# Performance work log

Measured on AMD Instinct MI355X. Metric: run time of the kernel, lower is better.

## Reference

```python
import jax, jax.numpy as jnp
import numpy as np

N_NODES = 50000
N_EDGES = 800000
NUM_GRAPHS = 1024
IN_DIM = 25
DIM = 64
STEPS = 3


def setup_inputs() -> dict:
    key = jax.random.key(0)
    ks = jax.random.split(key, 16)
    s = 0.1
    return {
        "x": jax.random.normal(ks[0], (N_NODES, IN_DIM), dtype=jnp.float32),
        "edge_index": jax.random.randint(ks[1], (2, N_EDGES), 0, N_NODES),
        "batch": jnp.sort(jax.random.randint(ks[2], (N_NODES,), 0, NUM_GRAPHS)),
        "W0": jax.random.normal(ks[3], (IN_DIM, DIM), dtype=jnp.float32) * s,
        "b0": jnp.zeros((DIM,), jnp.float32),
        "Wc": jax.random.normal(ks[4], (DIM, DIM), dtype=jnp.float32) * s,
        "bc": jnp.zeros((DIM,), jnp.float32),
        "Wih": jax.random.normal(ks[5], (4 * DIM, 2 * DIM), dtype=jnp.float32) * s,
        "Whh": jax.random.normal(ks[6], (4 * DIM, DIM), dtype=jnp.float32) * s,
        "bih": jnp.zeros((4 * DIM,), jnp.float32),
        "bhh": jnp.zeros((4 * DIM,), jnp.float32),
        "W1": jax.random.normal(ks[7], (2 * DIM, DIM), dtype=jnp.float32) * s,
        "b1": jnp.zeros((DIM,), jnp.float32),
        "W2": jax.random.normal(ks[8], (DIM, 1), dtype=jnp.float32) * s,
        "b2": jnp.zeros((1,), jnp.float32),
    }


def _lstm_cell(xin, h, c, Wih, Whh, bih, bhh):
    gates = xin @ Wih.T + h @ Whh.T + bih + bhh  # [B, 4*DIM]
    i, f, g, o = jnp.split(gates, 4, axis=-1)
    i, f, o = jax.nn.sigmoid(i), jax.nn.sigmoid(f), jax.nn.sigmoid(o)
    g = jnp.tanh(g)
    c = f * c + i * g
    h = o * jnp.tanh(c)
    return h, c


def reference(x, edge_index, batch, W0, b0, Wc, bc, Wih, Whh, bih, bhh, W1, b1, W2, b2):
    n = x.shape[0]
    # lin0 + relu
    h = jax.nn.relu(x @ W0 + b0)
    # GCNConv: x @ W, add self loops, symmetric normalization, scatter-add
    hw = h @ Wc
    loops = jnp.arange(n, dtype=edge_index.dtype)
    row = jnp.concatenate([edge_index[0], loops])  # sources
    col = jnp.concatenate([edge_index[1], loops])  # targets
    deg = jax.ops.segment_sum(jnp.ones_like(row, dtype=hw.dtype), col, num_segments=n)
    dinv = jnp.where(deg > 0, jax.lax.rsqrt(deg), 0.0)
    norm = dinv[row] * dinv[col]
    msg = hw[row] * norm[:, None]  # [E+N, DIM] gather
    agg = jax.ops.segment_sum(msg, col, num_segments=n) + bc
    h = jax.nn.relu(agg)
    # Set2Set pooling with LSTM, 3 processing steps
    B = NUM_GRAPHS
    q_star = jnp.zeros((B, 2 * DIM), h.dtype)
    hs = jnp.zeros((B, DIM), h.dtype)
    cs = jnp.zeros((B, DIM), h.dtype)
    for _ in range(STEPS):
        hs, cs = _lstm_cell(q_star, hs, cs, Wih, Whh, bih, bhh)
        q = hs  # [B, DIM]
        e = jnp.sum(h * q[batch], axis=-1)  # [N]
        emax = jax.ops.segment_max(e, batch, num_segments=B)
        a = jnp.exp(e - emax[batch])
        asum = jax.ops.segment_sum(a, batch, num_segments=B)
        a = a / asum[batch]
        r = jax.ops.segment_sum(a[:, None] * h, batch, num_segments=B)  # [B, DIM]
        q_star = jnp.concatenate([q, r], axis=-1)
    out = jax.nn.relu(q_star @ W1 + b1)
    out = out @ W2 + b2
    return out.reshape(-1)
```

## Files before the change

### kernel.cpp

```cpp
#include <hip/hip_runtime.h>
#include <hip/hip_fp16.h>
#include <math.h>

#define N_NODES 50000
#define N_EDGES 800000
#define NGRAPH  1024
#define IN_DIM  25
#define DIM     64

#define NBK 98
#define CAP 12288
#define NPB 128
#define NFILL (NBK * 4)
#define NBIN 391

__device__ inline float wsum(float v) {
#pragma unroll
  for (int off = 32; off > 0; off >>= 1) v += __shfl_xor(v, off, 64);
  return v;
}
__device__ inline int wsumi(int v) {
#pragma unroll
  for (int off = 32; off > 0; off >>= 1) v += __shfl_xor(v, off, 64);
  return v;
}
__device__ inline float sigmoidf(float x) { return 1.f / (1.f + expf(-x)); }

__global__ __launch_bounds__(256) void k_bin(const int* __restrict__ ei,
    int* __restrict__ gcur, int* __restrict__ pairs,
    const float* __restrict__ Wih, const float* __restrict__ Whh,
    float* __restrict__ WT) {
  __shared__ int lcnt[NBK];
  __shared__ int lbase[NBK];
  int t = threadIdx.x;
  if (blockIdx.x == NBIN) {
    for (int i = t; i < 3 * DIM * 4 * DIM; i += 256) {
      int k = i >> 8, tt = i & 255;
      WT[i] = (k < 2 * DIM) ? Wih[tt * 2 * DIM + k] : Whh[tt * DIM + (k - 2 * DIM)];
    }
    return;
  }
  int base = blockIdx.x * 2048;
  for (int i = t; i < NBK; i += 256) lcnt[i] = 0;
  __syncthreads();
  int rows[8], cols[8], rank[8];
#pragma unroll
  for (int k = 0; k < 8; k++) {
    int e = base + k * 256 + t;
    if (e < N_EDGES) {
      rows[k] = ei[e];
      cols[k] = ei[N_EDGES + e];
      rank[k] = atomicAdd(&lcnt[cols[k] >> 9], 1);
    } else {
      cols[k] = -1;
    }
  }
  __syncthreads();
  for (int i = t; i < NBK; i += 256)
    lbase[i] = lcnt[i] ? atomicAdd(&gcur[i], lcnt[i]) : 0;
  __syncthreads();
#pragma unroll
  for (int k = 0; k < 8; k++) {
    if (cols[k] >= 0) {
      int bkt = cols[k] >> 9;
      int pos = lbase[bkt] + rank[k];
      if (pos < CAP)
        pairs[(size_t)bkt * CAP + pos] = ((cols[k] & 511) << 16) | rows[k];
    }
  }
}

__global__ __launch_bounds__(256) void k_lin0(const float* __restrict__ x,
    const float* __restrict__ W0, const float* __restrict__ b0,
    const float* __restrict__ Wc, __half* __restrict__ hw16) {
  __shared__ float sx[64][IN_DIM + 1];
  __shared__ float sW0[IN_DIM][DIM];
  __shared__ float sh[64][DIM + 4];
  __shared__ float sWc[DIM][DIM];
  int t = threadIdx.x;
  int row0 = blockIdx.x * 64;
  for (int i = t; i < 64 * IN_DIM; i += 256) {
    int r = i / IN_DIM, k = i - r * IN_DIM;
    int row = row0 + r;
    sx[r][k] = (row < N_NODES) ? x[row * IN_DIM + k] : 0.f;
  }
  for (int i = t; i < IN_DIM * DIM; i += 256) sW0[i >> 6][i & 63] = W0[i];
  for (int i = t; i < DIM * DIM; i += 256) sWc[i >> 6][i & 63] = Wc[i];
  __syncthreads();
  int tc = (t & 15) * 4;
  int tr = (t >> 4) * 4;
  float acc[4][4];
  {
    float4 bb = *(const float4*)&b0[tc];
#pragma unroll
    for (int i = 0; i < 4; i++) {
      acc[i][0] = bb.x; acc[i][1] = bb.y; acc[i][2] = bb.z; acc[i][3] = bb.w;
    }
  }
#pragma unroll
  for (int k = 0; k < IN_DIM; k++) {
    float4 w = *(const float4*)&sW0[k][tc];
#pragma unroll
    for (int i = 0; i < 4; i++) {
      float a = sx[tr + i][k];
      acc[i][0] += a * w.x; acc[i][1] += a * w.y;
      acc[i][2] += a * w.z; acc[i][3] += a * w.w;
    }
  }
#pragma unroll
  for (int i = 0; i < 4; i++) {
    sh[tr + i][tc + 0] = fmaxf(acc[i][0], 0.f);
    sh[tr + i][tc + 1] = fmaxf(acc[i][1], 0.f);
    sh[tr + i][tc + 2] = fmaxf(acc[i][2], 0.f);
    sh[tr + i][tc + 3] = fmaxf(acc[i][3], 0.f);
  }
  __syncthreads();
#pragma unroll
  for (int i = 0; i < 4; i++) acc[i][0] = acc[i][1] = acc[i][2] = acc[i][3] = 0.f;
#pragma unroll 8
  for (int k = 0; k < DIM; k++) {
    float4 w = *(const float4*)&sWc[k][tc];
#pragma unroll
    for (int i = 0; i < 4; i++) {
      float a = sh[tr + i][k];
      acc[i][0] += a * w.x; acc[i][1] += a * w.y;
      acc[i][2] += a * w.z; acc[i][3] += a * w.w;
    }
  }
  float2* hwf2 = (float2*)hw16;
#pragma unroll
  for (int i = 0; i < 4; i++) {
    int row = row0 + tr + i;
    if (row < N_NODES) {
      float2 st;
      ((__half2*)&st)[0] = __floats2half2_rn(acc[i][0], acc[i][1]);
      ((__half2*)&st)[1] = __floats2half2_rn(acc[i][2], acc[i][3]);
      hwf2[(size_t)row * 16 + (t & 15)] = st;
    }
  }
}

__global__ __launch_bounds__(256) void k_fillcsr(const int* __restrict__ pairs,
    const int* __restrict__ gcur, int* __restrict__ cnt,
    float* __restrict__ dinv, int* __restrict__ adj, __half* __restrict__ hw16) {
  __shared__ int hist[NPB];
  __shared__ int sbase, sbef;
  int b = blockIdx.x;
  int cb = b >> 2, sub = b & 3;
  int t = threadIdx.x, wave = t >> 6, lane = t & 63;
  int lo = sub * NPB;
  int nb0 = cb * 512 + lo;
  if (t < NPB) hist[t] = 0;
  if (t == 0) { sbef = 0; sbase = 0; }
  __syncthreads();
  int ne = min(gcur[cb], CAP);
  const int* pp = pairs + (size_t)cb * CAP;
  int mybef = 0;
  for (int i = t; i < ne; i += 256) {
    int c = pp[i] >> 16;
    unsigned cl = (unsigned)(c - lo);
    if (cl < NPB) atomicAdd(&hist[cl], 1);
    mybef += (c < lo);
  }
  mybef = wsumi(mybef);
  if (lane == 0 && mybef) atomicAdd(&sbef, mybef);
  __syncthreads();
  __half2* hw2 = (__half2*)hw16;
  for (int n = wave; n < NPB; n += 4) {
    int node = nb0 + n;
    if (node >= N_NODES) break;
    float dv = rsqrtf((float)(hist[n] + 1));
    if (lane == 0) dinv[node] = dv;
    if (lane < 32) {
      __half2 v = hw2[(size_t)node * 32 + lane];
      float2 f = __half22float2(v);
      hw2[(size_t)node * 32 + lane] = __floats2half2_rn(f.x * dv, f.y * dv);
    }
  }
  if (t < 64) {
    int v = 0;
    for (int i = t; i < cb; i += 64) v += gcur[i];
    v = wsumi(v);
    if (t == 0) sbase = v;
  }
  __syncthreads();
  int basev = sbase + sbef;
  if (t < 64) {
    int v0 = hist[2 * t], v1 = hist[2 * t + 1];
    int loc = v0 + v1;
    int x = loc;
#pragma unroll
    for (int d = 1; d < 64; d <<= 1) {
      int y = __shfl_up(x, d, 64);
      if (t >= d) x += y;
    }
    int excl = basev + x - loc;
    hist[2 * t] = excl;
    hist[2 * t + 1] = excl + v0;
  }
  __syncthreads();
  if (t < NPB) {
    int node = nb0 + t;
    if (node < N_NODES) cnt[node] = hist[t];
  }
  if (b == NFILL - 1 && t == 0) cnt[N_NODES] = N_EDGES;
  __syncthreads();
  for (int i = t; i < ne; i += 256) {
    int p = pp[i];
    unsigned cl = (unsigned)((p >> 16) - lo);
    if (cl < NPB) {
      int slot = atomicAdd(&hist[cl], 1);
      adj[slot] = p & 0xFFFF;
    }
  }
}

__global__ __launch_bounds__(256) void k_gather(const int* __restrict__ adj,
    const int* __restrict__ cnt, const __half* __restrict__ hw16,
    const float* __restrict__ dinv, const float4* __restrict__ bc4,
    float4* __restrict__ h4) {
  int t = threadIdx.x;
  int lane = t & 63, wave = t >> 6;
  int q = lane >> 4, ql = lane & 15;
  int node = blockIdx.x * 16 + wave * 4 + q;
  if (node >= N_NODES) return;
  const float2* hwf2 = (const float2*)hw16;
  int s = cnt[node], eend = cnt[node + 1];
  float di = dinv[node];
  float4 a0 = make_float4(0.f, 0.f, 0.f, 0.f), a1 = a0, a2 = a0, a3 = a0;
  {
    float2 raw = hwf2[(size_t)node * 16 + ql];
    float2 f0 = __half22float2(((const __half2*)&raw)[0]);
    float2 f1 = __half22float2(((const __half2*)&raw)[1]);
    a0.x = f0.x; a0.y = f0.y; a0.z = f1.x; a0.w = f1.y;
  }
  int qb = q << 4;
  for (int cb = s; cb < eend; cb += 16) {
    int cn = min(16, eend - cb);
    int idx = (ql < cn) ? adj[cb + ql] : 0;
    int j = 0;
    for (; j + 4 <= cn; j += 4) {
      int r0 = __shfl(idx, qb + j, 64), r1 = __shfl(idx, qb + j + 1, 64);
      int r2 = __shfl(idx, qb + j + 2, 64), r3 = __shfl(idx, qb + j + 3, 64);
      float2 w0 = hwf2[(size_t)r0 * 16 + ql];
      float2 w1 = hwf2[(size_t)r1 * 16 + ql];
      float2 w2 = hwf2[(size_t)r2 * 16 + ql];
      float2 w3 = hwf2[(size_t)r3 * 16 + ql];
      float2 f;
      f = __half22float2(((const __half2*)&w0)[0]); a0.x += f.x; a0.y += f.y;
      f = __half22float2(((const __half2*)&w0)[1]); a0.z += f.x; a0.w += f.y;
      f = __half22float2(((const __half2*)&w1)[0]); a1.x += f.x; a1.y += f.y;
      f = __half22float2(((const __half2*)&w1)[1]); a1.z += f.x; a1.w += f.y;
      f = __half22float2(((const __half2*)&w2)[0]); a2.x += f.x; a2.y += f.y;
      f = __half22float2(((const __half2*)&w2)[1]); a2.z += f.x; a2.w += f.y;
      f = __half22float2(((const __half2*)&w3)[0]); a3.x += f.x; a3.y += f.y;
      f = __half22float2(((const __half2*)&w3)[1]); a3.z += f.x; a3.w += f.y;
    }
    for (; j < cn; j++) {
      int r = __shfl(idx, qb + j, 64);
      float2 w = hwf2[(size_t)r * 16 + ql];
      float2 f;
      f = __half22float2(((const __half2*)&w)[0]); a0.x += f.x; a0.y += f.y;
      f = __half22float2(((const __half2*)&w)[1]); a0.z += f.x; a0.w += f.y;
    }
  }
  float4 bb = bc4[ql];
  float4 o;
  o.x = fmaxf(((a0.x + a1.x) + (a2.x + a3.x)) * di + bb.x, 0.f);
  o.y = fmaxf(((a0.y + a1.y) + (a2.y + a3.y)) * di + bb.y, 0.f);
  o.z = fmaxf(((a0.z + a1.z) + (a2.z + a3.z)) * di + bb.z, 0.f);
  o.w = fmaxf(((a0.w + a1.w) + (a2.w + a3.w)) * di + bb.w, 0.f);
  h4[(size_t)node * 16 + ql] = o;
}

__global__ __launch_bounds__(256) void k_set2set(
    const float* __restrict__ h, const int* __restrict__ batch,
    const float* __restrict__ WT, const float* __restrict__ bih,
    const float* __restrict__ bhh, const float* __restrict__ W1,
    const float* __restrict__ b1, const float* __restrict__ W2,
    const float* __restrict__ b2, float* __restrict__ out) {
  int b = blockIdx.x, t = threadIdx.x;
  int wave = t >> 6, lane = t & 63;
  int q = lane >> 4, ql = lane & 15;
  int qid = (wave << 2) + q;
  __shared__ float qs[2 * DIM];
  __shared__ float hsl[DIM], csl[DIM];
  __shared__ float gates[4 * DIM];
  __shared__ float red[16 * DIM];
  __shared__ float lred[16], wmax[16];
  __shared__ int seg[2];
  const float4* h4 = (const float4*)h;
  if (t < 2) {
    int g = b + t;
    int lo = 0, hi = N_NODES;
    if (g == NGRAPH) lo = N_NODES;
    else while (lo < hi) { int mid = (lo + hi) >> 1; if (batch[mid] < g) lo = mid + 1; else hi = mid; }
    seg[t] = lo;
  }
  if (t < 2 * DIM) qs[t] = 0.f;
  if (t < DIM) { hsl[t] = 0.f; csl[t] = 0.f; }
  __syncthreads();
  int s = seg[0], eend = seg[1];
  float bsum = bih[t] + bhh[t];
  for (int step = 0; step < 3; step++) {
    float g = bsum;
    if (step > 0) {
      const float* wp = WT + t;
      float g1 = 0.f;
#pragma unroll 8
      for (int k = 0; k < 2 * DIM; k += 2) {
        g += qs[k] * wp[k * 4 * DIM];
        g1 += qs[k + 1] * wp[(k + 1) * 4 * DIM];
      }
#pragma unroll 8
      for (int k = 0; k < DIM; k += 2) {
        g += hsl[k] * wp[(2 * DIM + k) * 4 * DIM];
        g1 += hsl[k + 1] * wp[(2 * DIM + k + 1) * 4 * DIM];
      }
      g += g1;
    }
    gates[t] = g;
    __syncthreads();
    if (t < DIM) {
      float ig = sigmoidf(gates[t]);
      float fg = sigmoidf(gates[DIM + t]);
      float gg = tanhf(gates[2 * DIM + t]);
      float og = sigmoidf(gates[3 * DIM + t]);
      float c = fg * csl[t] + ig * gg;
      csl[t] = c;
      float hh = og * tanhf(c);
      hsl[t] = hh;
      qs[t] = hh;
    }
    __syncthreads();
    float4 qf = *(const float4*)&hsl[4 * ql];
    float m_w = -INFINITY, l_w = 0.f;
    float4 racc = make_float4(0.f, 0.f, 0.f, 0.f);
    for (int j = s + qid; j < eend; j += 16) {
      float4 hv = h4[(size_t)j * 16 + ql];
      float p = hv.x * qf.x + hv.y * qf.y + hv.z * qf.z + hv.w * qf.w;
#pragma unroll
      for (int off = 1; off < 16; off <<= 1) p += __shfl_xor(p, off, 64);
      float m_new = fmaxf(m_w, p);
      float scale = __expf(m_w - m_new);
      float a = __expf(p - m_new);
      racc.x = racc.x * scale + a * hv.x;
      racc.y = racc.y * scale + a * hv.y;
      racc.z = racc.z * scale + a * hv.z;
      racc.w = racc.w * scale + a * hv.w;
      l_w = l_w * scale + a;
      m_w = m_new;
    }
    *(float4*)&red[qid * DIM + 4 * ql] = racc;
    if (ql == 0) { lred[qid] = l_w; wmax[qid] = m_w; }
    __syncthreads();
    if (t < DIM) {
      float m_b = -1e30f;
      for (int i = 0; i < 16; i++) m_b = fmaxf(m_b, wmax[i]);
      float r = 0.f, l = 0.f;
      for (int i = 0; i < 16; i++) {
        float e = __expf(wmax[i] - m_b);
        r += red[i * DIM + t] * e;
        l += lred[i] * e;
      }
      qs[DIM + t] = (l > 0.f) ? r / l : 0.f;
    }
    __syncthreads();
  }
  if (t < DIM) {
    float acc = b1[t];
#pragma unroll
    for (int k = 0; k < 2 * DIM; k++) acc += qs[k] * W1[k * DIM + t];
    acc = fmaxf(acc, 0.f);
    float v = wsum(acc * W2[t]);
    if (t == 0) out[b] = v + b2[0];
  }
}

extern "C" void kernel_launch(void* const* d_in, const int* in_sizes, int n_in,
                              void* d_out, int out_size, void* d_ws, size_t ws_size,
                              hipStream_t stream) {
  const float* x    = (const float*)d_in[0];
  const int*   ei   = (const int*)d_in[1];
  const int*   batch= (const int*)d_in[2];
  const float* W0   = (const float*)d_in[3];
  const float* b0   = (const float*)d_in[4];
  const float* Wc   = (const float*)d_in[5];
  const float* bc   = (const float*)d_in[6];
  const float* Wih  = (const float*)d_in[7];
  const float* Whh  = (const float*)d_in[8];
  const float* bih  = (const float*)d_in[9];
  const float* bhh  = (const float*)d_in[10];
  const float* W1   = (const float*)d_in[11];
  const float* b1   = (const float*)d_in[12];
  const float* W2   = (const float*)d_in[13];
  const float* b2   = (const float*)d_in[14];
  float* out = (float*)d_out;

  float* ws    = (float*)d_ws;
  __half* hw16 = (__half*)ws;
  float* h     = ws + (size_t)N_NODES * DIM / 2;
  float* dinv  = h + (size_t)N_NODES * DIM;
  float* WT    = dinv + N_NODES;
  int* cnt     = (int*)(WT + 3 * DIM * 4 * DIM);
  int* adj     = cnt + N_NODES + 2;
  int* gcur    = adj + N_EDGES;
  int* pairs   = gcur + NBK + 2;

  hipMemsetAsync(gcur, 0, NBK * sizeof(int), stream);
  k_bin<<<NBIN + 1, 256, 0, stream>>>(ei, gcur, pairs, Wih, Whh, WT);
  k_lin0<<<(N_NODES + 63) / 64, 256, 0, stream>>>(x, W0, b0, Wc, hw16);
  k_fillcsr<<<NFILL, 256, 0, stream>>>(pairs, gcur, cnt, dinv, adj, hw16);
  k_gather<<<(N_NODES + 15) / 16, 256, 0, stream>>>(adj, cnt, hw16, dinv,
                                                    (const float4*)bc, (float4*)h);
  k_set2set<<<NGRAPH, 256, 0, stream>>>(h, batch, WT, bih, bhh, W1, b1, W2, b2, out);
}
```

Before: 222.4 us.

## Locally sort bin writes, fold dinv scaling into lin0, store h in fp16

k_bin now sorts each block's edges by bucket in shared memory before writing, so global stores to the per-bucket pairs array are contiguous runs instead of scattered. k_fillcsr runs before k_lin0 and only computes dinv; k_lin0 applies the dinv scale when it writes hw16, which removes the read-modify-write pass over hw16. The GCN output h is stored in fp16 instead of fp32, halving the bytes k_set2set reads. The cost is extra shared memory and a scan in k_bin, and reduced precision in h.

```diff
diff --git a/kernel.cpp b/kernel.cpp
--- a/kernel.cpp
+++ b/kernel.cpp
@@ -30,8 +30,10 @@
     int* __restrict__ gcur, int* __restrict__ pairs,
     const float* __restrict__ Wih, const float* __restrict__ Whh,
     float* __restrict__ WT) {
-  __shared__ int lcnt[NBK];
+  __shared__ int hist[NBK];
+  __shared__ int sbase[NBK];
   __shared__ int lbase[NBK];
+  __shared__ int sorted[2048];
   int t = threadIdx.x;
   if (blockIdx.x == NBIN) {
     for (int i = t; i < 3 * DIM * 4 * DIM; i += 256) {
@@ -41,38 +43,125 @@
     return;
   }
   int base = blockIdx.x * 2048;
-  for (int i = t; i < NBK; i += 256) lcnt[i] = 0;
-  __syncthreads();
-  int rows[8], cols[8], rank[8];
+  for (int i = t; i < NBK; i += 256) hist[i] = 0;
+  __syncthreads();
+  int pk[8], bkt[8], rank[8];
 #pragma unroll
   for (int k = 0; k < 8; k++) {
     int e = base + k * 256 + t;
     if (e < N_EDGES) {
-      rows[k] = ei[e];
-      cols[k] = ei[N_EDGES + e];
-      rank[k] = atomicAdd(&lcnt[cols[k] >> 9], 1);
+      int row = ei[e];
+      int col = ei[N_EDGES + e];
+      int b = col >> 9;
+      bkt[k] = b;
+      rank[k] = atomicAdd(&hist[b], 1);
+      pk[k] = (b << 25) | ((col & 511) << 16) | row;
     } else {
-      cols[k] = -1;
-    }
-  }
-  __syncthreads();
+      bkt[k] = -1;
+    }
+  }
+  __syncthreads();
+  if (t < 64) {
+    int i0 = 2 * t, i1 = 2 * t + 1;
+    int v0 = (i0 < NBK) ? hist[i0] : 0;
+    int v1 = (i1 < NBK) ? hist[i1] : 0;
+    int loc = v0 + v1, x = loc;
+#pragma unroll
+    for (int d = 1; d < 64; d <<= 1) {
+      int y = __shfl_up(x, d, 64);
+      if (t >= d) x += y;
+    }
+    int excl = x - loc;
+    if (i0 < NBK) sbase[i0] = excl;
+    if (i1 < NBK) sbase[i1] = excl + v0;
+  }
+  __syncthreads();
+#pragma unroll
+  for (int k = 0; k < 8; k++)
+    if (bkt[k] >= 0) sorted[sbase[bkt[k]] + rank[k]] = pk[k];
   for (int i = t; i < NBK; i += 256)
-    lbase[i] = lcnt[i] ? atomicAdd(&gcur[i], lcnt[i]) : 0;
-  __syncthreads();
-#pragma unroll
-  for (int k = 0; k < 8; k++) {
-    if (cols[k] >= 0) {
-      int bkt = cols[k] >> 9;
-      int pos = lbase[bkt] + rank[k];
-      if (pos < CAP)
-        pairs[(size_t)bkt * CAP + pos] = ((cols[k] & 511) << 16) | rows[k];
+    lbase[i] = hist[i] ? atomicAdd(&gcur[i], hist[i]) : 0;
+  __syncthreads();
+  int ntot = min(2048, N_EDGES - base);
+  for (int i = t; i < ntot; i += 256) {
+    int p = sorted[i];
+    int b = ((unsigned)p) >> 25;
+    int gpos = lbase[b] + (i - sbase[b]);
+    if (gpos < CAP) pairs[(size_t)b * CAP + gpos] = p & 0x1FFFFFF;
+  }
+}
+
+__global__ __launch_bounds__(256) void k_fillcsr(const int* __restrict__ pairs,
+    const int* __restrict__ gcur, int* __restrict__ cnt,
+    float* __restrict__ dinv, int* __restrict__ adj) {
+  __shared__ int hist[NPB];
+  __shared__ int sbase, sbef;
+  int b = blockIdx.x;
+  int cb = b >> 2, sub = b & 3;
+  int t = threadIdx.x, lane = t & 63;
+  int lo = sub * NPB;
+  int nb0 = cb * 512 + lo;
+  if (t < NPB) hist[t] = 0;
+  if (t == 0) { sbef = 0; sbase = 0; }
+  __syncthreads();
+  int ne = min(gcur[cb], CAP);
+  const int* pp = pairs + (size_t)cb * CAP;
+  int mybef = 0;
+  for (int i = t; i < ne; i += 256) {
+    int c = pp[i] >> 16;
+    unsigned cl = (unsigned)(c - lo);
+    if (cl < NPB) atomicAdd(&hist[cl], 1);
+    mybef += (c < lo);
+  }
+  mybef = wsumi(mybef);
+  if (lane == 0 && mybef) atomicAdd(&sbef, mybef);
+  __syncthreads();
+  if (t < NPB) {
+    int node = nb0 + t;
+    if (node < N_NODES) dinv[node] = rsqrtf((float)(hist[t] + 1));
+  }
+  if (t < 64) {
+    int v = 0;
+    for (int i = t; i < cb; i += 64) v += gcur[i];
+    v = wsumi(v);
+    if (t == 0) sbase = v;
+  }
+  __syncthreads();
+  int basev = sbase + sbef;
+  if (t < 64) {
+    int v0 = hist[2 * t], v1 = hist[2 * t + 1];
+    int loc = v0 + v1;
+    int x = loc;
+#pragma unroll
+    for (int d = 1; d < 64; d <<= 1) {
+      int y = __shfl_up(x, d, 64);
+      if (t >= d) x += y;
+    }
+    int excl = basev + x - loc;
+    hist[2 * t] = excl;
+    hist[2 * t + 1] = excl + v0;
+  }
+  __syncthreads();
+  if (t < NPB) {
+    int node = nb0 + t;
+    if (node < N_NODES) cnt[node] = hist[t];
+  }
+  if (b == NFILL - 1 && t == 0) cnt[N_NODES] = N_EDGES;
+  __syncthreads();
+  for (int i = t; i < ne; i += 256) {
+    int p = pp[i];
+    unsigned cl = (unsigned)((p >> 16) - lo);
+    if (cl < NPB) {
+      int slot = atomicAdd(&hist[cl], 1);
+      adj[slot] = p & 0xFFFF;
     }
   }
 }
 
 __global__ __launch_bounds__(256) void k_lin0(const float* __restrict__ x,
     const float* __restrict__ W0, const float* __restrict__ b0,
-    const float* __restrict__ Wc, __half* __restrict__ hw16) {
+    const float* __restrict__ Wc, const float* __restrict__ dinv,
+    __half* __restrict__ hw16) {
   __shared__ float sx[64][IN_DIM + 1];
   __shared__ float sW0[IN_DIM][DIM];
   __shared__ float sh[64][DIM + 4];
@@ -132,85 +221,11 @@
   for (int i = 0; i < 4; i++) {
     int row = row0 + tr + i;
     if (row < N_NODES) {
+      float dv = dinv[row];
       float2 st;
-      ((__half2*)&st)[0] = __floats2half2_rn(acc[i][0], acc[i][1]);
-      ((__half2*)&st)[1] = __floats2half2_rn(acc[i][2], acc[i][3]);
+      ((__half2*)&st)[0] = __floats2half2_rn(acc[i][0] * dv, acc[i][1] * dv);
+      ((__half2*)&st)[1] = __floats2half2_rn(acc[i][2] * dv, acc[i][3] * dv);
       hwf2[(size_t)row * 16 + (t & 15)] = st;
-    }
-  }
-}
-
-__global__ __launch_bounds__(256) void k_fillcsr(const int* __restrict__ pairs,
-    const int* __restrict__ gcur, int* __restrict__ cnt,
-    float* __restrict__ dinv, int* __restrict__ adj, __half* __restrict__ hw16) {
-  __shared__ int hist[NPB];
-  __shared__ int sbase, sbef;
-  int b = blockIdx.x;
-  int cb = b >> 2, sub = b & 3;
-  int t = threadIdx.x, wave = t >> 6, lane = t & 63;
-  int lo = sub * NPB;
-  int nb0 = cb * 512 + lo;
-  if (t < NPB) hist[t] = 0;
-  if (t == 0) { sbef = 0; sbase = 0; }
-  __syncthreads();
-  int ne = min(gcur[cb], CAP);
-  const int* pp = pairs + (size_t)cb * CAP;
-  int mybef = 0;
-  for (int i = t; i < ne; i += 256) {
-    int c = pp[i] >> 16;
-    unsigned cl = (unsigned)(c - lo);
-    if (cl < NPB) atomicAdd(&hist[cl], 1);
-    mybef += (c < lo);
-  }
-  mybef = wsumi(mybef);
-  if (lane == 0 && mybef) atomicAdd(&sbef, mybef);
-  __syncthreads();
-  __half2* hw2 = (__half2*)hw16;
-  for (int n = wave; n < NPB; n += 4) {
-    int node = nb0 + n;
-    if (node >= N_NODES) break;
-    float dv = rsqrtf((float)(hist[n] + 1));
-    if (lane == 0) dinv[node] = dv;
-    if (lane < 32) {
-      __half2 v = hw2[(size_t)node * 32 + lane];
-      float2 f = __half22float2(v);
-      hw2[(size_t)node * 32 + lane] = __floats2half2_rn(f.x * dv, f.y * dv);
-    }
-  }
-  if (t < 64) {
-    int v = 0;
-    for (int i = t; i < cb; i += 64) v += gcur[i];
-    v = wsumi(v);
-    if (t == 0) sbase = v;
-  }
-  __syncthreads();
-  int basev = sbase + sbef;
-  if (t < 64) {
-    int v0 = hist[2 * t], v1 = hist[2 * t + 1];
-    int loc = v0 + v1;
-    int x = loc;
-#pragma unroll
-    for (int d = 1; d < 64; d <<= 1) {
-      int y = __shfl_up(x, d, 64);
-      if (t >= d) x += y;
-    }
-    int excl = basev + x - loc;
-    hist[2 * t] = excl;
-    hist[2 * t + 1] = excl + v0;
-  }
-  __syncthreads();
-  if (t < NPB) {
-    int node = nb0 + t;
-    if (node < N_NODES) cnt[node] = hist[t];
-  }
-  if (b == NFILL - 1 && t == 0) cnt[N_NODES] = N_EDGES;
-  __syncthreads();
-  for (int i = t; i < ne; i += 256) {
-    int p = pp[i];
-    unsigned cl = (unsigned)((p >> 16) - lo);
-    if (cl < NPB) {
-      int slot = atomicAdd(&hist[cl], 1);
-      adj[slot] = p & 0xFFFF;
     }
   }
 }
@@ -218,7 +233,7 @@
 __global__ __launch_bounds__(256) void k_gather(const int* __restrict__ adj,
     const int* __restrict__ cnt, const __half* __restrict__ hw16,
     const float* __restrict__ dinv, const float4* __restrict__ bc4,
-    float4* __restrict__ h4) {
+    __half* __restrict__ h16) {
   int t = threadIdx.x;
   int lane = t & 63, wave = t >> 6;
   int q = lane >> 4, ql = lane & 15;
@@ -265,16 +280,18 @@
     }
   }
   float4 bb = bc4[ql];
-  float4 o;
-  o.x = fmaxf(((a0.x + a1.x) + (a2.x + a3.x)) * di + bb.x, 0.f);
-  o.y = fmaxf(((a0.y + a1.y) + (a2.y + a3.y)) * di + bb.y, 0.f);
-  o.z = fmaxf(((a0.z + a1.z) + (a2.z + a3.z)) * di + bb.z, 0.f);
-  o.w = fmaxf(((a0.w + a1.w) + (a2.w + a3.w)) * di + bb.w, 0.f);
-  h4[(size_t)node * 16 + ql] = o;
+  float ox = fmaxf(((a0.x + a1.x) + (a2.x + a3.x)) * di + bb.x, 0.f);
+  float oy = fmaxf(((a0.y + a1.y) + (a2.y + a3.y)) * di + bb.y, 0.f);
+  float oz = fmaxf(((a0.z + a1.z) + (a2.z + a3.z)) * di + bb.z, 0.f);
+  float ow = fmaxf(((a0.w + a1.w) + (a2.w + a3.w)) * di + bb.w, 0.f);
+  float2 st;
+  ((__half2*)&st)[0] = __floats2half2_rn(ox, oy);
+  ((__half2*)&st)[1] = __floats2half2_rn(oz, ow);
+  ((float2*)h16)[(size_t)node * 16 + ql] = st;
 }
 
 __global__ __launch_bounds__(256) void k_set2set(
-    const float* __restrict__ h, const int* __restrict__ batch,
+    const __half* __restrict__ h16, const int* __restrict__ batch,
     const float* __restrict__ WT, const float* __restrict__ bih,
     const float* __restrict__ bhh, const float* __restrict__ W1,
     const float* __restrict__ b1, const float* __restrict__ W2,
@@ -289,7 +306,7 @@
   __shared__ float red[16 * DIM];
   __shared__ float lred[16], wmax[16];
   __shared__ int seg[2];
-  const float4* h4 = (const float4*)h;
+  const float2* h2 = (const float2*)h16;
   if (t < 2) {
     int g = b + t;
     int lo = 0, hi = N_NODES;
@@ -337,17 +354,19 @@
     float m_w = -INFINITY, l_w = 0.f;
     float4 racc = make_float4(0.f, 0.f, 0.f, 0.f);
     for (int j = s + qid; j < eend; j += 16) {
-      float4 hv = h4[(size_t)j * 16 + ql];
-      float p = hv.x * qf.x + hv.y * qf.y + hv.z * qf.z + hv.w * qf.w;
+      float2 raw = h2[(size_t)j * 16 + ql];
+      float2 f0 = __half22float2(((const __half2*)&raw)[0]);
+      float2 f1 = __half22float2(((const __half2*)&raw)[1]);
+      float p = f0.x * qf.x + f0.y * qf.y + f1.x * qf.z + f1.y * qf.w;
 #pragma unroll
       for (int off = 1; off < 16; off <<= 1) p += __shfl_xor(p, off, 64);
       float m_new = fmaxf(m_w, p);
       float scale = __expf(m_w - m_new);
       float a = __expf(p - m_new);
-      racc.x = racc.x * scale + a * hv.x;
-      racc.y = racc.y * scale + a * hv.y;
-      racc.z = racc.z * scale + a * hv.z;
-      racc.w = racc.w * scale + a * hv.w;
+      racc.x = racc.x * scale + a * f0.x;
+      racc.y = racc.y * scale + a * f0.y;
+      racc.z = racc.z * scale + a * f1.x;
+      racc.w = racc.w * scale + a * f1.y;
       l_w = l_w * scale + a;
       m_w = m_new;
     }
@@ -397,10 +416,9 @@
   const float* b2   = (const float*)d_in[14];
   float* out = (float*)d_out;
 
-  float* ws    = (float*)d_ws;
-  __half* hw16 = (__half*)ws;
-  float* h     = ws + (size_t)N_NODES * DIM / 2;
-  float* dinv  = h + (size_t)N_NODES * DIM;
+  __half* hw16 = (__half*)d_ws;
+  __half* h16  = hw16 + (size_t)N_NODES * DIM;
+  float* dinv  = (float*)(h16 + (size_t)N_NODES * DIM);
   float* WT    = dinv + N_NODES;
   int* cnt     = (int*)(WT + 3 * DIM * 4 * DIM);
   int* adj     = cnt + N_NODES + 2;
@@ -409,9 +427,9 @@
 
   hipMemsetAsync(gcur, 0, NBK * sizeof(int), stream);
   k_bin<<<NBIN + 1, 256, 0, stream>>>(ei, gcur, pairs, Wih, Whh, WT);
-  k_lin0<<<(N_NODES + 63) / 64, 256, 0, stream>>>(x, W0, b0, Wc, hw16);
-  k_fillcsr<<<NFILL, 256, 0, stream>>>(pairs, gcur, cnt, dinv, adj, hw16);
+  k_fillcsr<<<NFILL, 256, 0, stream>>>(pairs, gcur, cnt, dinv, adj);
+  k_lin0<<<(N_NODES + 63) / 64, 256, 0, stream>>>(x, W0, b0, Wc, dinv, hw16);
   k_gather<<<(N_NODES + 15) / 16, 256, 0, stream>>>(adj, cnt, hw16, dinv,
-                                                    (const float4*)bc, (float4*)h);
-  k_set2set<<<NGRAPH, 256, 0, stream>>>(h, batch, WT, bih, bhh, W1, b1, W2, b2, out);
-}
+                                                    (const float4*)bc, h16);
+  k_set2set<<<NGRAPH, 256, 0, stream>>>(h16, batch, WT, bih, bhh, W1, b1, W2, b2, out);
+}
```

After: 209.4 us. 5.9% less time.
